# Performance work log

Hardware: AMD Instinct MI355X
Metric: run time of the kernel (lower is better)

## Reference

```python
import jax, jax.numpy as jnp
import numpy as np

NUM_E = 20000   # entities
NUM_R = 200     # relations (rel table has 2*NUM_R rows)
H = 200         # h_dim
TD = 48         # t_dim (UnionTimeEncode: two halves of 24)
HD = TD // 2
L_HIST = 32     # padded per-(batch,k) history list length
HIS_K = 3
N_HIST = 3      # len(his_list_g)
N_LAYERS = 2    # RGCN layers (config.num_layers)
E = 200000      # edges per historical graph
BATCH = 512


def setup_inputs() -> dict:
    key = jax.random.key(0)
    ks = jax.random.split(key, 32)
    nrm = lambda k, shape, s=0.05: (jax.random.normal(k, shape, jnp.float32) * s)
    inp = {}
    # graph / index inputs (int)
    inp['src'] = jax.random.randint(ks[0], (N_HIST, E), 0, NUM_E, jnp.int32)
    inp['dst'] = jax.random.randint(ks[1], (N_HIST, E), 0, NUM_E, jnp.int32)
    inp['etype'] = jax.random.randint(ks[2], (N_HIST, E), 0, 2 * NUM_R, jnp.int32)
    inp['data'] = jax.random.randint(ks[3], (BATCH, 4), 0, NUM_R, jnp.int32)  # s,r,o,t
    inp['his_idx'] = jax.random.randint(ks[4], (BATCH, HIS_K, L_HIST), 0, NUM_E, jnp.int32)
    inp['his_len'] = jax.random.randint(ks[5], (BATCH, HIS_K), 0, L_HIST + 1, jnp.int32)
    # parameters (float)
    inp['ent'] = nrm(ks[6], (NUM_E, H), 0.5)          # EntEmb.ent (normal init)
    inp['loop_weight'] = nrm(ks[7], (H, H))           # EntEmb self-loop weight
    inp['rel'] = nrm(ks[8], (2 * NUM_R, H), 0.5)
    # UnionTimeEncode params (AbsTimeEncode v=0 + CosTimeEncode)
    basis = (1.0 / 10 ** np.linspace(0.0, 9.0, HD)).astype(np.float32)
    inp['abs_freq'] = jnp.asarray(basis)
    inp['abs_phase'] = jnp.zeros((HD,), jnp.float32)
    inp['cos_freq'] = jnp.asarray(basis)
    inp['cos_phase'] = jnp.zeros((HD,), jnp.float32)
    # RGCN (RE-GCN style Union-RGCN layer: msg=(h_src+rel_e)@Wn, mean agg, self-loop)
    inp['Wn'] = nrm(ks[9], (N_LAYERS, H, H))
    inp['Ws'] = nrm(ks[10], (N_LAYERS, H, H))
    # GRUCell (PyTorch layout)
    inp['W_ih'] = nrm(ks[11], (3 * H, H + TD))
    inp['W_hh'] = nrm(ks[12], (3 * H, H))
    inp['b_ih'] = jnp.zeros((3 * H,), jnp.float32)
    inp['b_hh'] = jnp.zeros((3 * H,), jnp.float32)
    # attention fusion
    inp['Wb_w'] = nrm(ks[13], (H, 3 * H + TD))
    inp['Wb_b'] = jnp.zeros((H,), jnp.float32)
    inp['Wc_w'] = nrm(ks[14], (1, H))
    inp['Wc_b'] = jnp.zeros((1,), jnp.float32)
    # decoder (MLP query @ entity table)
    inp['Wd_w'] = nrm(ks[15], (H, 3 * H))
    inp['Wd_b'] = jnp.zeros((H,), jnp.float32)
    return inp


def _l2n(x, eps=1e-12):
    # F.normalize: x / max(||x||, eps)
    n = jnp.linalg.norm(x, axis=-1, keepdims=True)
    return x / jnp.maximum(n, eps)


def reference(src, dst, etype, data, his_idx, his_len,
              ent, loop_weight, rel, abs_freq, abs_phase, cos_freq, cos_phase,
              Wn, Ws, W_ih, W_hh, b_ih, b_hh, Wb_w, Wb_b, Wc_w, Wc_b, Wd_w, Wd_b):
    def tenc(t):  # t: [N,1] float -> [N,TD]
        a = jnp.tanh((t + 1.0) * abs_freq + abs_phase)   # AbsTimeEncode(act=tanh)
        c = jnp.cos(t * cos_freq + cos_phase)            # CosTimeEncode
        return jnp.concatenate([a, c], axis=1)

    s_i, r_i = data[:, 0], data[:, 1]
    ent_e = ent @ loop_weight                  # EntEmb self-loop (dropout=identity, eval)
    rel_n = _l2n(rel)
    prev = _l2n(ent_e)                         # g_list[0]
    tim_cnt = N_HIST
    ones_e = jnp.ones((E,), jnp.float32)
    for i in range(N_HIST):                    # python loop over fixed #graphs
        si, di, ei = src[i], dst[i], etype[i]
        deg = jax.ops.segment_sum(ones_e, di, num_segments=NUM_E)         # in-degree
        inv = 1.0 / jnp.maximum(deg, 1.0)
        # g.update_all(copy_src, mean): zero in-degree nodes -> 0
        agg = jax.ops.segment_sum(prev[si], di, num_segments=NUM_E) * inv[:, None]
        h = _l2n(jnp.where(deg[:, None] > 0, agg, 0.0))
        tim_cnt -= 1
        tim = jnp.where(deg > 0, float(tim_cnt), 100.0)[:, None]
        te = tenc(tim)                                                     # [NUM_E,TD]
        for l in range(N_LAYERS):              # RGCN
            msg = (h[si] + rel_n[ei]) @ Wn[l]                              # [E,H]
            nagg = jax.ops.segment_sum(msg, di, num_segments=NUM_E) * inv[:, None]
            h = jax.nn.relu(nagg + h @ Ws[l])
        h = _l2n(h)
        # GRUCell(cat([h, te]), prev)
        gi = jnp.concatenate([h, te], axis=1) @ W_ih.T + b_ih
        gh = prev @ W_hh.T + b_hh
        ir, iz, iN = jnp.split(gi, 3, axis=1)
        hr, hz, hN = jnp.split(gh, 3, axis=1)
        rg = jax.nn.sigmoid(ir + hr)
        zg = jax.nn.sigmoid(iz + hz)
        ng = jnp.tanh(iN + rg * hN)
        prev = _l2n((1.0 - zg) * ng + zg * prev)
    out = prev

    q_s, q_r = out[s_i], rel_n[r_i]
    tim_cnt = min(N_HIST, HIS_K)
    s_embs, atts = [], []
    pos = jnp.arange(L_HIST)[None, :]
    for k in range(min(N_HIST, HIS_K)):
        tim_cnt -= 1
        ln = his_len[:, k]
        mask = (pos < ln[:, None]).astype(jnp.float32)                     # [B,L]
        # sparse one-hot mm + divide by length
        tmp = jnp.einsum('blh,bl->bh', out[his_idx[:, k, :]], mask)
        tmp = _l2n(tmp / jnp.maximum(ln, 1).astype(jnp.float32)[:, None])
        tim = jnp.where(ln > 0, float(tim_cnt), 100.0)[:, None]
        te = tenc(tim)                                                     # [B,TD]
        s_embs.append(tmp)
        a = jax.nn.relu(jnp.concatenate([q_s, q_r, tmp, te], 1) @ Wb_w.T + Wb_b)
        atts.append(a @ Wc_w.T + Wc_b)                                     # [B,1]
    att = jax.nn.softmax(jnp.stack(atts, axis=1), axis=1)                  # [B,K,1]
    out2 = jnp.sum(jnp.stack(s_embs, axis=1) * att, axis=1)                # bmm fusion
    # decoder: MLP query scored against all entity states
    q = jax.nn.relu(jnp.concatenate([q_s, q_r, out2], 1) @ Wd_w.T + Wd_b)
    return q @ out.T                                                       # [B,NUM_E]
```

## Files before the change

kernel.cpp:

```cpp
#include <hip/hip_runtime.h>
#include <hip/hip_bf16.h>

#define NUM_E   20000
#define H_DIM   200
#define TD_DIM  48
#define HD_DIM  24
#define L_HIST  32
#define N_HIST  3
#define E_EDGES 200000
#define BATCH   512


__device__ inline float wave_sum64(float x) {
    #pragma unroll
    for (int m = 1; m < 64; m <<= 1) x += __shfl_xor(x, m);
    return x;
}

__device__ inline ushort f2bf(float f) {
    unsigned u = __float_as_uint(f);
    u += 0x7fffu + ((u >> 16) & 1u);
    return (ushort)(u >> 16);
}
__device__ inline float bf2f(ushort u) {
    return __uint_as_float(((unsigned)u) << 16);
}
__device__ inline float4 bf4_to_f4(ushort4 v) {
    return (float4){bf2f(v.x), bf2f(v.y), bf2f(v.z), bf2f(v.w)};
}

__global__ void fill_i32(int* __restrict__ p, long n, int v) {
    long i = (long)blockIdx.x * blockDim.x + threadIdx.x;
    if (i < n) p[i] = v;
}

__global__ void bias_sum(float* __restrict__ bsum, const float* __restrict__ b_ih,
                         const float* __restrict__ b_hh) {
    int j = blockIdx.x * 256 + threadIdx.x;
    if (j < 600) bsum[j] = b_ih[j] + b_hh[j];
}

__global__ void cvt_bf16_k(ushort* __restrict__ o, const float* __restrict__ in, long n) {
    long i = (long)blockIdx.x * 256 + threadIdx.x;
    if (i < n) o[i] = f2bf(in[i]);
}

__global__ void make_lo(ushort* __restrict__ lo, const float* __restrict__ x,
                        const ushort* __restrict__ hi, long n) {
    long i = (long)blockIdx.x * 256 + threadIdx.x;
    if (i < n) lo[i] = f2bf(x[i] - bf2f(hi[i]));
}

__global__ void tcvt_bf16_k(ushort* __restrict__ o, const float* __restrict__ in, int R, int C) {
    int i = blockIdx.x * 256 + threadIdx.x;
    if (i >= R * C) return;
    int r = i / C, c = i - r * C;
    o[(size_t)c * R + r] = f2bf(in[i]);
}

struct Segs {
    const float* A[4];
    const float* B[4];
    int lda[4], ldb[4], Ks[4];
    int nseg, Ktot;
};

__device__ inline void seg_find(const Segs& sg, int gk, int& s, int& loc) {
    s = 0; loc = gk;
    #pragma unroll
    for (int t = 0; t < 3; t++) {
        if (s + 1 < sg.nseg && loc >= sg.Ks[s]) { loc -= sg.Ks[s]; s++; }
    }
}

__global__ __launch_bounds__(256) void sgemm_splitk(
    float* __restrict__ P, const Segs sg, int M, int N, int nbx, int nby,
    int KS, int tpc)
{
    __shared__ float As[32][68];
    __shared__ float Bs[32][68];

    int tot = nbx * nby;
    int tot_all = tot * KS;
    int chunk = (tot_all + 7) >> 3;
    int v = (int)(blockIdx.x & 7) * chunk + (int)(blockIdx.x >> 3);
    if (v >= tot_all) return;
    int kc = v / tot;
    int tile = v - kc * tot;
    int by = tile / nbx, bx = tile - by * nbx;
    const int bn = bx * 64;
    const int bm = by * 64;
    const int tid = threadIdx.x;
    const int m0 = (tid >> 4) * 4;
    const int n0 = (tid & 15) * 4;

    float acc[4][4];
    #pragma unroll
    for (int i = 0; i < 4; i++)
        #pragma unroll
        for (int j = 0; j < 4; j++) acc[i][j] = 0.f;

    const int Ktot = sg.Ktot;
    const int ntile = (Ktot + 31) / 32;
    const int kt0 = kc * tpc;
    const int kt1 = min(ntile, kt0 + tpc);

    const int a_m  = tid & 31;
    const int a_k4 = (tid >> 5) * 4;
    const int b1_n = tid & 63;
    const int b1_k = (tid >> 6) * 4;

    float4 ra[2], rb[2];
    auto loadA = [&](int k0) {
        int gk = k0 + a_k4;
        bool kin = gk < Ktot;
        int s = 0, loc = 0;
        if (kin) seg_find(sg, gk, s, loc);
        const float* Ab = sg.A[s];
        const int lda = sg.lda[s];
        #pragma unroll
        for (int r = 0; r < 2; r++) {
            int row = bm + a_m + 32 * r;
            float4 vv = {0.f, 0.f, 0.f, 0.f};
            if (kin && row < M) vv = *(const float4*)(Ab + (size_t)row * lda + loc);
            ra[r] = vv;
        }
    };
    auto loadB = [&](int k0) {
        #pragma unroll
        for (int r = 0; r < 2; r++) {
            int k4 = b1_k + 16 * r;
            int gk = k0 + k4;
            bool kin = gk < Ktot;
            int s = 0, loc = 0;
            if (kin) seg_find(sg, gk, s, loc);
            const float* Bb = sg.B[s];
            const int ldb = sg.ldb[s];
            int gn = bn + b1_n;
            float4 vv = {0.f, 0.f, 0.f, 0.f};
            if (kin && gn < N) vv = *(const float4*)(Bb + (size_t)gn * ldb + loc);
            rb[r] = vv;
        }
    };

    if (kt0 < kt1) {
        loadA(kt0 * 32); loadB(kt0 * 32);
        for (int t = kt0; t < kt1; t++) {
            #pragma unroll
            for (int r = 0; r < 2; r++) {
                int m = a_m + 32 * r;
                As[a_k4 + 0][m] = ra[r].x;
                As[a_k4 + 1][m] = ra[r].y;
                As[a_k4 + 2][m] = ra[r].z;
                As[a_k4 + 3][m] = ra[r].w;
            }
            #pragma unroll
            for (int r = 0; r < 2; r++) {
                int k4 = b1_k + 16 * r;
                Bs[k4 + 0][b1_n] = rb[r].x;
                Bs[k4 + 1][b1_n] = rb[r].y;
                Bs[k4 + 2][b1_n] = rb[r].z;
                Bs[k4 + 3][b1_n] = rb[r].w;
            }
            __syncthreads();
            if (t + 1 < kt1) { loadA((t + 1) * 32); loadB((t + 1) * 32); }
            #pragma unroll 8
            for (int kk = 0; kk < 32; kk++) {
                float4 b = *(float4*)&Bs[kk][n0];
                float4 av = *(float4*)&As[kk][m0];
                float a[4] = {av.x, av.y, av.z, av.w};
                #pragma unroll
                for (int i = 0; i < 4; i++) {
                    acc[i][0] += a[i] * b.x;
                    acc[i][1] += a[i] * b.y;
                    acc[i][2] += a[i] * b.z;
                    acc[i][3] += a[i] * b.w;
                }
            }
            __syncthreads();
        }
    }

    int col = bn + n0;
    if (col < N) {
        #pragma unroll
        for (int i = 0; i < 4; i++) {
            int row = bm + m0 + i;
            if (row < M) {
                float4 o = {acc[i][0], acc[i][1], acc[i][2], acc[i][3]};
                *(float4*)(P + ((size_t)kc * M + row) * N + col) = o;
            }
        }
    }
}

__global__ void reduce_relu(float* __restrict__ out, const float* __restrict__ P,
                            const float* __restrict__ bias, int MN, int N, int KS)
{
    int i = blockIdx.x * 256 + threadIdx.x;
    if (i >= MN) return;
    float s = bias[i % N];
    for (int k = 0; k < KS; k++) s += P[(size_t)k * MN + i];
    out[i] = fmaxf(s, 0.f);
}

__global__ void reduce_relu_split(ushort* __restrict__ qhi, ushort* __restrict__ qlo,
                                  const float* __restrict__ P, const float* __restrict__ bias,
                                  int MN, int N, int KS)
{
    int i = blockIdx.x * 256 + threadIdx.x;
    if (i >= MN) return;
    float s = bias[i % N];
    for (int k = 0; k < KS; k++) s += P[(size_t)k * MN + i];
    s = fmaxf(s, 0.f);
    ushort h = f2bf(s);
    qhi[i] = h;
    qlo[i] = f2bf(s - bf2f(h));
}

typedef __attribute__((ext_vector_type(8))) short bfrag;
typedef __attribute__((ext_vector_type(4))) float ffrag;

struct BfSegs {
    const ushort* A[3];
    const ushort* B[3];
    int lda[3], ldb[3], Ks[3];
    int nseg, Ktot;
};

__device__ inline void bseg_find(const BfSegs& sg, int gk, int& s, int& loc) {
    s = 0; loc = gk;
    #pragma unroll
    for (int t = 0; t < 2; t++) {
        if (s + 1 < sg.nseg && loc >= sg.Ks[s]) { loc -= sg.Ks[s]; s++; }
    }
}

struct GemmDesc {
    BfSegs sg;
    float* C;
    ushort* Cb;
    const float* bias;
    int M, N, ldc;
    int act, flags, order;
    int nbx, nby, blk0, nblk;
};

struct MultiArgs {
    GemmDesc d[3];
    int nd;
    int tot;
};

template<int DI>
__device__ __forceinline__ void gemm_body(const MultiArgs& ma, int v,
                                          ushort* __restrict__ Als,
                                          ushort* __restrict__ Bls)
{
    const GemmDesc& D = ma.d[DI];
    const BfSegs& sg = D.sg;
    const int tile = v - D.blk0;
    int by, bx;
    if (D.order == 0) { by = tile / D.nbx; bx = tile - by * D.nbx; }
    else              { bx = tile / D.nby; by = tile - bx * D.nby; }
    const int bm = by * 64, bn = bx * 64;
    const int M = D.M, N = D.N;

    const int tid  = threadIdx.x;
    const int lane = tid & 63;
    const int w    = tid >> 6;
    const int wm   = (w & 1) * 2;
    const int wn   = (w >> 1) * 2;

    ffrag acc[2][2];
    #pragma unroll
    for (int i = 0; i < 2; i++)
        #pragma unroll
        for (int j = 0; j < 2; j++) acc[i][j] = (ffrag){0.f, 0.f, 0.f, 0.f};

    const int Ktot = sg.Ktot;
    const int nkt = (Ktot + 63) >> 6;

    int a_m[2], a_kq[2], a_wc[2];
    #pragma unroll
    for (int i = 0; i < 2; i++) {
        int c = i * 256 + tid;
        a_m[i] = c & 63; a_kq[i] = c >> 6;
        a_wc[i] = ((a_m[i] >> 4) * 2 + (a_kq[i] >> 2)) * 64 + (a_kq[i] & 3) * 16 + (a_m[i] & 15);
    }
    int b_n[2], b_kq[2], b_wc[2];
    #pragma unroll
    for (int i = 0; i < 2; i++) {
        int c = i * 256 + tid;
        b_n[i] = c & 63; b_kq[i] = c >> 6;
        b_wc[i] = ((b_n[i] >> 4) * 2 + (b_kq[i] >> 2)) * 64 + (b_kq[i] & 3) * 16 + (b_n[i] & 15);
    }

    uint4 ra[2], rb[2];
    auto loadA = [&](int k0) {
        #pragma unroll
        for (int i = 0; i < 2; i++) {
            int gk = k0 + a_kq[i] * 8;
            int row = bm + a_m[i];
            uint4 vv = {0u, 0u, 0u, 0u};
            if (gk < Ktot && row < M) {
                int s, loc; bseg_find(sg, gk, s, loc);
                vv = *(const uint4*)(sg.A[s] + (size_t)row * sg.lda[s] + loc);
            }
            ra[i] = vv;
        }
    };
    auto loadB = [&](int k0) {
        #pragma unroll
        for (int i = 0; i < 2; i++) {
            int gk = k0 + b_kq[i] * 8;
            int gn = bn + b_n[i];
            uint4 vv = {0u, 0u, 0u, 0u};
            if (gk < Ktot && gn < N) {
                int s, loc; bseg_find(sg, gk, s, loc);
                vv = *(const uint4*)(sg.B[s] + (size_t)gn * sg.ldb[s] + loc);
            }
            rb[i] = vv;
        }
    };

    loadA(0); loadB(0);

    for (int t = 0; t < nkt; t++) {
        #pragma unroll
        for (int i = 0; i < 2; i++) *(uint4*)(&Als[a_wc[i] * 8]) = ra[i];
        #pragma unroll
        for (int i = 0; i < 2; i++) *(uint4*)(&Bls[b_wc[i] * 8]) = rb[i];
        __syncthreads();

        if (t + 1 < nkt) { loadA((t + 1) << 6); loadB((t + 1) << 6); }

        #pragma unroll
        for (int kt = 0; kt < 2; kt++) {
            bfrag af[2], bf[2];
            #pragma unroll
            for (int i = 0; i < 2; i++)
                af[i] = *(const bfrag*)(&Als[(((wm + i) * 2 + kt) * 64 + lane) * 8]);
            #pragma unroll
            for (int j = 0; j < 2; j++)
                bf[j] = *(const bfrag*)(&Bls[(((wn + j) * 2 + kt) * 64 + lane) * 8]);
            #pragma unroll
            for (int i = 0; i < 2; i++)
                #pragma unroll
                for (int j = 0; j < 2; j++)
                    acc[i][j] = __builtin_amdgcn_mfma_f32_16x16x32_bf16(af[i], bf[j], acc[i][j], 0, 0, 0);
        }
        __syncthreads();
    }

    const int rbase = (lane >> 4) * 4;
    const int cl = lane & 15;
    #pragma unroll
    for (int j = 0; j < 2; j++) {
        int col = bn + (wn + j) * 16 + cl;
        if (col >= N) continue;
        float bv = D.bias ? D.bias[col] : 0.f;
        #pragma unroll
        for (int i = 0; i < 2; i++) {
            int mrow = bm + (wm + i) * 16 + rbase;
            #pragma unroll
            for (int r = 0; r < 4; r++) {
                int row = mrow + r;
                if (row < M) {
                    float o = acc[i][j][r] + bv;
                    if (D.act == 1) o = fmaxf(o, 0.f);
                    else if (D.act == 2) o = 1.f / (1.f + expf(-o));
                    if (D.flags & 1) D.C[(size_t)row * D.ldc + col] = o;
                    if (D.flags & 2) D.Cb[(size_t)row * D.ldc + col] = f2bf(o);
                }
            }
        }
    }
}

__global__ __launch_bounds__(256) void mfma_multi(MultiArgs ma)
{
    __shared__ __align__(16) ushort Als[4096];
    __shared__ __align__(16) ushort Bls[4096];

    int tot = ma.tot;
    int chunk = (tot + 7) >> 3;
    int v = (int)(blockIdx.x & 7) * chunk + (int)(blockIdx.x >> 3);
    if (v >= tot) return;

    int di = 0;
    if (ma.nd > 1 && v >= ma.d[1].blk0) di = 1;
    if (ma.nd > 2 && v >= ma.d[2].blk0) di = 2;

    if (di == 0)      gemm_body<0>(ma, v, Als, Bls);
    else if (di == 1) gemm_body<1>(ma, v, Als, Bls);
    else              gemm_body<2>(ma, v, Als, Bls);
}


__global__ void count_dst3(const int* __restrict__ dst, int* __restrict__ cnt) {
    long e = (long)blockIdx.x * 256 + threadIdx.x;
    if (e < (long)N_HIST * E_EDGES) {
        int g = (int)(e / E_EDGES);
        atomicAdd(&cnt[g * NUM_E + dst[e]], 1);
    }
}

__global__ __launch_bounds__(1024) void scan_rows3(
    const int* __restrict__ cnt_all, int* __restrict__ row_start_all,
    int* __restrict__ cursor_all, float* __restrict__ degf_all,
    float* __restrict__ invd_all)
{
    __shared__ int part[1024];
    const int g = blockIdx.x;
    const int* cnt = cnt_all + g * NUM_E;
    int* row_start  = row_start_all + g * (NUM_E + 4);
    int* cursor     = cursor_all + g * NUM_E;
    float* degf     = degf_all + g * NUM_E;
    float* invd     = invd_all + g * NUM_E;

    const int CH = (NUM_E + 1023) / 1024;
    int t = threadIdx.x;
    int base = t * CH;
    int local[32];
    int s = 0;
    for (int j = 0; j < CH; j++) {
        int idx = base + j;
        int c = (idx < NUM_E) ? cnt[idx] : 0;
        local[j] = s; s += c;
    }
    part[t] = s;
    __syncthreads();
    for (int off = 1; off < 1024; off <<= 1) {
        int vv = (t >= off) ? part[t - off] : 0;
        __syncthreads();
        part[t] += vv;
        __syncthreads();
    }
    int pre = (t == 0) ? 0 : part[t - 1];
    for (int j = 0; j < CH; j++) {
        int idx = base + j;
        if (idx < NUM_E) {
            int rs = pre + local[j];
            row_start[idx] = rs;
            cursor[idx] = rs;
            int c = cnt[idx];
            degf[idx] = (float)c;
            invd[idx] = 1.f / fmaxf((float)c, 1.f);
        }
    }
    if (t == 1023) row_start[NUM_E] = part[1023];
}

__global__ void build_perm3(const int* __restrict__ src, const int* __restrict__ dst,
                            const int* __restrict__ etype, int* __restrict__ cursor_all,
                            int* __restrict__ ssrc_all, int* __restrict__ setype_all)
{
    long e = (long)blockIdx.x * 256 + threadIdx.x;
    if (e >= (long)N_HIST * E_EDGES) return;
    int g = (int)(e / E_EDGES);
    int pos = atomicAdd(&cursor_all[g * NUM_E + dst[e]], 1);
    ssrc_all[(long)g * E_EDGES + pos]   = src[e];
    setype_all[(long)g * E_EDGES + pos] = etype[e];
}


__global__ __launch_bounds__(256) void seg_gather_norm_bf(
    ushort* __restrict__ bh, const ushort* __restrict__ bprev,
    const int* __restrict__ ssrc, const int* __restrict__ row_start,
    const float* __restrict__ invd)
{
    int v = blockIdx.x * 4 + (threadIdx.x >> 6);
    int lane = threadIdx.x & 63;
    if (v >= NUM_E) return;
    int s0 = row_start[v], s1 = row_start[v + 1];
    bool act = lane < 50;
    float4 acc = {0.f, 0.f, 0.f, 0.f};
    int j = s0;
    for (; j + 1 < s1; j += 2) {
        int sa = ssrc[j], sb = ssrc[j + 1];
        if (act) {
            float4 xa = bf4_to_f4(*(const ushort4*)(bprev + (long)sa * H_DIM + lane * 4));
            float4 xb = bf4_to_f4(*(const ushort4*)(bprev + (long)sb * H_DIM + lane * 4));
            acc.x += xa.x + xb.x; acc.y += xa.y + xb.y;
            acc.z += xa.z + xb.z; acc.w += xa.w + xb.w;
        }
    }
    if (j < s1) {
        int sa = ssrc[j];
        if (act) {
            float4 xa = bf4_to_f4(*(const ushort4*)(bprev + (long)sa * H_DIM + lane * 4));
            acc.x += xa.x; acc.y += xa.y; acc.z += xa.z; acc.w += xa.w;
        }
    }
    float iv = invd[v];
    acc.x *= iv; acc.y *= iv; acc.z *= iv; acc.w *= iv;
    float ss = act ? (acc.x*acc.x + acc.y*acc.y + acc.z*acc.z + acc.w*acc.w) : 0.f;
    ss = wave_sum64(ss);
    float r = 1.f / fmaxf(sqrtf(ss), 1e-12f);
    if (act) {
        ushort4 ob = {f2bf(acc.x * r), f2bf(acc.y * r), f2bf(acc.z * r), f2bf(acc.w * r)};
        *(ushort4*)(bh + (long)v * H_DIM + lane * 4) = ob;
    }
}

__global__ __launch_bounds__(256) void seg_gather_layer_bf(
    ushort* __restrict__ btmp, const ushort* __restrict__ bh, const ushort* __restrict__ brel,
    const int* __restrict__ ssrc, const int* __restrict__ setype,
    const int* __restrict__ row_start, const float* __restrict__ invd)
{
    int v = blockIdx.x * 4 + (threadIdx.x >> 6);
    int lane = threadIdx.x & 63;
    if (v >= NUM_E) return;
    int s0 = row_start[v], s1 = row_start[v + 1];
    bool act = lane < 50;
    float4 acc = {0.f, 0.f, 0.f, 0.f};
    int j = s0;
    for (; j + 1 < s1; j += 2) {
        int sa = ssrc[j], ta = setype[j];
        int sb = ssrc[j + 1], tb = setype[j + 1];
        if (act) {
            float4 xa = bf4_to_f4(*(const ushort4*)(bh   + (long)sa * H_DIM + lane * 4));
            float4 ya = bf4_to_f4(*(const ushort4*)(brel + (long)ta * H_DIM + lane * 4));
            float4 xb = bf4_to_f4(*(const ushort4*)(bh   + (long)sb * H_DIM + lane * 4));
            float4 yb = bf4_to_f4(*(const ushort4*)(brel + (long)tb * H_DIM + lane * 4));
            acc.x += (xa.x + ya.x) + (xb.x + yb.x);
            acc.y += (xa.y + ya.y) + (xb.y + yb.y);
            acc.z += (xa.z + ya.z) + (xb.z + yb.z);
            acc.w += (xa.w + ya.w) + (xb.w + yb.w);
        }
    }
    if (j < s1) {
        int s = ssrc[j];
        int t = setype[j];
        if (act) {
            float4 x = bf4_to_f4(*(const ushort4*)(bh   + (long)s * H_DIM + lane * 4));
            float4 y = bf4_to_f4(*(const ushort4*)(brel + (long)t * H_DIM + lane * 4));
            acc.x += x.x + y.x; acc.y += x.y + y.y;
            acc.z += x.z + y.z; acc.w += x.w + y.w;
        }
    }
    float iv = invd[v];
    if (act) {
        ushort4 ob = {f2bf(acc.x * iv), f2bf(acc.y * iv), f2bf(acc.z * iv), f2bf(acc.w * iv)};
        *(ushort4*)(btmp + (long)v * H_DIM + lane * 4) = ob;
    }
}


__global__ __launch_bounds__(256) void l2norm_rows4(
    float* __restrict__ out, ushort* __restrict__ bout,
    const float* __restrict__ in, int nrows)
{
    int v = blockIdx.x * 4 + (threadIdx.x >> 6);
    int lane = threadIdx.x & 63;
    if (v >= nrows) return;
    bool act = lane < 50;
    float4 x = {0.f, 0.f, 0.f, 0.f};
    if (act) x = *(const float4*)(in + (long)v * H_DIM + lane * 4);
    float ss = x.x*x.x + x.y*x.y + x.z*x.z + x.w*x.w;
    ss = wave_sum64(ss);
    float r = 1.f / fmaxf(sqrtf(ss), 1e-12f);
    if (act) {
        long base = (long)v * H_DIM + lane * 4;
        float4 o = {x.x * r, x.y * r, x.z * r, x.w * r};
        *(float4*)(out + base) = o;
        if (bout) {
            ushort4 ob = {f2bf(o.x), f2bf(o.y), f2bf(o.z), f2bf(o.w)};
            *(ushort4*)(bout + base) = ob;
        }
    }
}

__global__ __launch_bounds__(256) void l2norm_bf4(ushort* __restrict__ b, int nrows)
{
    int v = blockIdx.x * 4 + (threadIdx.x >> 6);
    int lane = threadIdx.x & 63;
    if (v >= nrows) return;
    bool act = lane < 50;
    float4 x = {0.f, 0.f, 0.f, 0.f};
    long base = (long)v * H_DIM + lane * 4;
    if (act) x = bf4_to_f4(*(const ushort4*)(b + base));
    float ss = x.x*x.x + x.y*x.y + x.z*x.z + x.w*x.w;
    ss = wave_sum64(ss);
    float r = 1.f / fmaxf(sqrtf(ss), 1e-12f);
    if (act) {
        ushort4 ob = {f2bf(x.x * r), f2bf(x.y * r), f2bf(x.z * r), f2bf(x.w * r)};
        *(ushort4*)(b + base) = ob;
    }
}

__global__ void tenc_table3(ushort* __restrict__ tbl, const float* __restrict__ af,
                            const float* __restrict__ ap, const float* __restrict__ cf,
                            const float* __restrict__ cp)
{
    int j = blockIdx.x * 256 + threadIdx.x;
    if (j >= 384) return;
    int g = j >> 7;
    int r = j & 127;
    int half = r >> 6;
    int jj = r & 63;
    if (jj >= TD_DIM) return;
    float tcnt = (float)(N_HIST - 1 - g);
    float t = half ? 100.0f : tcnt;
    float val;
    if (jj < HD_DIM) val = tanhf((t + 1.f) * af[jj] + ap[jj]);
    else             val = cosf(t * cf[jj - HD_DIM] + cp[jj - HD_DIM]);
    tbl[g * 128 + half * 64 + jj] = f2bf(val);
}

__global__ void tenc_fill3(ushort* __restrict__ bte3, const float* __restrict__ degf_all,
                           const ushort* __restrict__ tbl)
{
    long idx = (long)blockIdx.x * 256 + threadIdx.x;
    if (idx >= (long)N_HIST * NUM_E * 6) return;
    int g = (int)(idx / (NUM_E * 6));
    int rem = (int)(idx - (long)g * NUM_E * 6);
    int v = rem / 6, c = rem - v * 6;
    int base = (degf_all[g * NUM_E + v] > 0.f) ? 0 : 64;
    *(uint4*)(bte3 + ((long)g * NUM_E + v) * TD_DIM + c * 8) =
        *(const uint4*)(tbl + g * 128 + base + c * 8);
}

__global__ __launch_bounds__(256) void gru_fused(
    float* __restrict__ prev, ushort* __restrict__ bprev, const float* __restrict__ rz,
    const float* __restrict__ iN, const float* __restrict__ hN)
{
    int v = blockIdx.x * 4 + (threadIdx.x >> 6);
    int lane = threadIdx.x & 63;
    if (v >= NUM_E) return;
    bool act = lane < 50;
    long b200 = (long)v * H_DIM + lane * 4;
    long b400 = (long)v * 400 + lane * 4;
    float4 o = {0.f, 0.f, 0.f, 0.f};
    if (act) {
        float4 r4 = *(const float4*)(rz + b400);
        float4 z4 = *(const float4*)(rz + b400 + 200);
        float4 n4 = *(const float4*)(iN + b200);
        float4 g4 = *(const float4*)(hN + b200);
        float4 p4 = *(const float4*)(prev + b200);
        float ngx = tanhf(n4.x + r4.x * g4.x);
        float ngy = tanhf(n4.y + r4.y * g4.y);
        float ngz = tanhf(n4.z + r4.z * g4.z);
        float ngw = tanhf(n4.w + r4.w * g4.w);
        o.x = (1.f - z4.x) * ngx + z4.x * p4.x;
        o.y = (1.f - z4.y) * ngy + z4.y * p4.y;
        o.z = (1.f - z4.z) * ngz + z4.z * p4.z;
        o.w = (1.f - z4.w) * ngw + z4.w * p4.w;
    }
    float ss = o.x*o.x + o.y*o.y + o.z*o.z + o.w*o.w;
    ss = wave_sum64(ss);
    float r = 1.f / fmaxf(sqrtf(ss), 1e-12f);
    if (act) {
        float4 wv = {o.x * r, o.y * r, o.z * r, o.w * r};
        *(float4*)(prev + b200) = wv;
        ushort4 ob = {f2bf(wv.x), f2bf(wv.y), f2bf(wv.z), f2bf(wv.w)};
        *(ushort4*)(bprev + b200) = ob;
    }
}


__global__ void gather_qs_qr3(float* __restrict__ qs3, float* __restrict__ qr3,
                              const float* __restrict__ out, const float* __restrict__ reln,
                              const int* __restrict__ data)
{
    long i = (long)blockIdx.x * 256 + threadIdx.x;
    if (i >= (long)BATCH * H_DIM) return;
    int b = (int)(i / H_DIM), j = (int)(i % H_DIM);
    float vs = out[(long)data[b * 4 + 0] * H_DIM + j];
    float vr = reln[(long)data[b * 4 + 1] * H_DIM + j];
    const long S = (long)BATCH * H_DIM;
    qs3[i] = vs; qs3[i + S] = vs; qs3[i + 2*S] = vs;
    qr3[i] = vr; qr3[i + S] = vr; qr3[i + 2*S] = vr;
}

__global__ __launch_bounds__(64) void semb_kernel(
    float* __restrict__ semb, const float* __restrict__ out,
    const int* __restrict__ his_idx, const int* __restrict__ his_len)
{
    int b = blockIdx.x, k = blockIdx.y;
    int lane = threadIdx.x;
    int ln = his_len[b * 3 + k];
    if (ln > L_HIST) ln = L_HIST;
    float vals[4] = {0.f, 0.f, 0.f, 0.f};
    for (int l = 0; l < ln; l++) {
        int idx = his_idx[((long)b * 3 + k) * L_HIST + l];
        #pragma unroll
        for (int t = 0; t < 4; t++) {
            int j = lane + t * 64;
            if (j < H_DIM) vals[t] += out[(long)idx * H_DIM + j];
        }
    }
    float scale = 1.f / fmaxf((float)ln, 1.f);
    float ss = 0.f;
    #pragma unroll
    for (int t = 0; t < 4; t++) { vals[t] *= scale; ss += vals[t] * vals[t]; }
    ss = wave_sum64(ss);
    float r = 1.f / fmaxf(sqrtf(ss), 1e-12f);
    #pragma unroll
    for (int t = 0; t < 4; t++) {
        int j = lane + t * 64;
        if (j < H_DIM) semb[((long)k * BATCH + b) * H_DIM + j] = vals[t] * r;
    }
}

__global__ void tenc_batch(float* __restrict__ teb, const int* __restrict__ his_len,
                           const float* __restrict__ af, const float* __restrict__ ap,
                           const float* __restrict__ cf, const float* __restrict__ cp)
{
    int idx = blockIdx.x * 256 + threadIdx.x;
    if (idx >= 3 * BATCH * TD_DIM) return;
    int k = idx / (BATCH * TD_DIM);
    int rem = idx - k * (BATCH * TD_DIM);
    int b = rem / TD_DIM, j = rem % TD_DIM;
    int ln = his_len[b * 3 + k];
    float t = (ln > 0) ? (float)(2 - k) : 100.0f;
    float val;
    if (j < HD_DIM) val = tanhf((t + 1.f) * af[j] + ap[j]);
    else            val = cosf(t * cf[j - HD_DIM] + cp[j - HD_DIM]);
    teb[idx] = val;
}

__global__ __launch_bounds__(256) void att_logits_rows(
    float* __restrict__ atts, const float* __restrict__ a,
    const float* __restrict__ Wc_w, const float* __restrict__ Wc_b)
{
    int row = blockIdx.x * 4 + (threadIdx.x >> 6);
    int lane = threadIdx.x & 63;
    if (row >= 3 * BATCH) return;
    int k = row >> 9;
    int b = row & 511;
    float s = 0.f;
    for (int j = lane; j < H_DIM; j += 64) s += a[(long)row * H_DIM + j] * Wc_w[j];
    s = wave_sum64(s);
    if (lane == 0) atts[b * 3 + k] = s + Wc_b[0];
}

__global__ void softmax_out2(float* __restrict__ out2, const float* __restrict__ atts,
                             const float* __restrict__ semb)
{
    long i = (long)blockIdx.x * 256 + threadIdx.x;
    if (i >= (long)BATCH * H_DIM) return;
    int b = (int)(i / H_DIM), j = (int)(i % H_DIM);
    float l0 = atts[b * 3 + 0], l1 = atts[b * 3 + 1], l2 = atts[b * 3 + 2];
    float m = fmaxf(l0, fmaxf(l1, l2));
    float e0 = expf(l0 - m), e1 = expf(l1 - m), e2 = expf(l2 - m);
    float s = e0 + e1 + e2;
    float v = (e0 * semb[((long)0 * BATCH + b) * H_DIM + j] +
               e1 * semb[((long)1 * BATCH + b) * H_DIM + j] +
               e2 * semb[((long)2 * BATCH + b) * H_DIM + j]) / s;
    out2[i] = v;
}


extern "C" void kernel_launch(void* const* d_in, const int* in_sizes, int n_in,
                              void* d_out, int out_size, void* d_ws, size_t ws_size,
                              hipStream_t stream)
{
    (void)in_sizes; (void)n_in; (void)out_size; (void)ws_size;

    const int*   src     = (const int*)d_in[0];
    const int*   dst     = (const int*)d_in[1];
    const int*   etype   = (const int*)d_in[2];
    const int*   data    = (const int*)d_in[3];
    const int*   his_idx = (const int*)d_in[4];
    const int*   his_len = (const int*)d_in[5];
    const float* ent     = (const float*)d_in[6];
    const float* loop_w  = (const float*)d_in[7];
    const float* rel     = (const float*)d_in[8];
    const float* af      = (const float*)d_in[9];
    const float* ap      = (const float*)d_in[10];
    const float* cf      = (const float*)d_in[11];
    const float* cp      = (const float*)d_in[12];
    const float* Wn      = (const float*)d_in[13];
    const float* Ws      = (const float*)d_in[14];
    const float* W_ih    = (const float*)d_in[15];
    const float* W_hh    = (const float*)d_in[16];
    const float* b_ih    = (const float*)d_in[17];
    const float* b_hh    = (const float*)d_in[18];
    const float* Wb_w    = (const float*)d_in[19];
    const float* Wb_b    = (const float*)d_in[20];
    const float* Wc_w    = (const float*)d_in[21];
    const float* Wc_b    = (const float*)d_in[22];
    const float* Wd_w    = (const float*)d_in[23];
    const float* Wd_b    = (const float*)d_in[24];
    float* out_p = (float*)d_out;

    float* wp = (float*)d_ws;
    size_t off = 0;
    auto alloc = [&](size_t n) {
        size_t n4 = (n + 3) & ~(size_t)3;
        float* p = wp + off; off += n4; return p;
    };
    const long nE200 = (long)NUM_E * H_DIM;
    float* prev   = alloc(nE200);
    float* h1     = alloc(nE200);
    float* tmp    = alloc(nE200);
    float* rz     = out_p;
    ushort* bh0   = (ushort*)alloc(nE200 / 2);
    ushort* bh1   = (ushort*)alloc(nE200 / 2);
    ushort* btmp  = (ushort*)alloc(nE200 / 2);
    ushort* bprev = (ushort*)alloc(nE200 / 2);
    ushort* plo   = (ushort*)alloc(nE200 / 2);
    ushort* bte3  = (ushort*)alloc((size_t)N_HIST * NUM_E * TD_DIM / 2);
    ushort* brel  = (ushort*)alloc(400 * H_DIM / 2);
    ushort* bW_ih = (ushort*)alloc(600 * 248 / 2);
    ushort* bW_hh = (ushort*)alloc(600 * 200 / 2);
    ushort* bWn_t = (ushort*)alloc(2 * 200 * 200 / 2);
    ushort* bWs_t = (ushort*)alloc(2 * 200 * 200 / 2);
    ushort* bLp_t = (ushort*)alloc(200 * 200 / 2);
    ushort* qhi   = (ushort*)alloc(BATCH * H_DIM / 2);
    ushort* qlo   = (ushort*)alloc(BATCH * H_DIM / 2);
    ushort* ttbl  = (ushort*)alloc(256);
    float* degf   = alloc(3 * NUM_E);
    float* invd   = alloc(3 * NUM_E);
    float* reln   = alloc(400 * H_DIM);
    float* bsum   = alloc(1024);
    float* qs3    = alloc(3 * BATCH * H_DIM);
    float* qr3    = alloc(3 * BATCH * H_DIM);
    float* semb   = alloc(3 * BATCH * H_DIM);
    float* teb    = alloc(3 * BATCH * TD_DIM);
    float* abuf   = alloc(3 * BATCH * H_DIM);
    float* atts   = alloc(2048);
    float* out2   = alloc(BATCH * H_DIM);
    int* cnt       = (int*)alloc(3 * NUM_E);
    int* row_start = (int*)alloc(3 * (NUM_E + 4));
    int* cursor    = (int*)alloc(3 * NUM_E);
    int* ssrc      = (int*)alloc(3L * E_EDGES);
    int* setype    = (int*)alloc(3L * E_EDGES);

    auto nblk = [](long n) { return (unsigned)((n + 255) / 256); };

    auto bseg1 = [](const ushort* A, int la, const ushort* B, int lb, int K) {
        BfSegs s{}; s.A[0]=A; s.lda[0]=la; s.B[0]=B; s.ldb[0]=lb; s.Ks[0]=K;
        s.nseg=1; s.Ktot=K; return s;
    };
    auto bseg2 = [](const ushort* A0, int la0, const ushort* B0, int lb0, int K0,
                    const ushort* A1, int la1, const ushort* B1, int lb1, int K1) {
        BfSegs s{}; s.A[0]=A0; s.lda[0]=la0; s.B[0]=B0; s.ldb[0]=lb0; s.Ks[0]=K0;
        s.A[1]=A1; s.lda[1]=la1; s.B[1]=B1; s.ldb[1]=lb1; s.Ks[1]=K1;
        s.nseg=2; s.Ktot=K0+K1; return s;
    };
    auto bseg3 = [](const ushort* A0, int la0, const ushort* B0, int lb0, int K0,
                    const ushort* A1, int la1, const ushort* B1, int lb1, int K1,
                    const ushort* A2, int la2, const ushort* B2, int lb2, int K2) {
        BfSegs s{}; s.A[0]=A0; s.lda[0]=la0; s.B[0]=B0; s.ldb[0]=lb0; s.Ks[0]=K0;
        s.A[1]=A1; s.lda[1]=la1; s.B[1]=B1; s.ldb[1]=lb1; s.Ks[1]=K1;
        s.A[2]=A2; s.lda[2]=la2; s.B[2]=B2; s.ldb[2]=lb2; s.Ks[2]=K2;
        s.nseg=3; s.Ktot=K0+K1+K2; return s;
    };

    auto desc = [](const BfSegs& sg, float* C, ushort* Cb, const float* bias,
                   int M, int N, int ldc, int act, int flags, int order) {
        GemmDesc D{}; D.sg=sg; D.C=C; D.Cb=Cb; D.bias=bias;
        D.M=M; D.N=N; D.ldc=ldc; D.act=act; D.flags=flags; D.order=order;
        D.nbx=(N+63)>>6; D.nby=(M+63)>>6; D.nblk=D.nbx*D.nby; D.blk0=0;
        return D;
    };
    auto launch_multi = [&](GemmDesc* ds, int nd) {
        MultiArgs ma{};
        int tot = 0;
        for (int i = 0; i < nd; i++) { ds[i].blk0 = tot; tot += ds[i].nblk; ma.d[i] = ds[i]; }
        ma.nd = nd; ma.tot = tot;
        unsigned grid = (unsigned)(((tot + 7) >> 3) << 3);
        mfma_multi<<<grid, 256, 0, stream>>>(ma);
    };

    auto seg3 = [](const float* A0, int la0, const float* B0, int lb0, int K0,
                   const float* A1, int la1, const float* B1, int lb1, int K1,
                   const float* A2, int la2, const float* B2, int lb2, int K2) {
        Segs s{}; s.A[0]=A0; s.lda[0]=la0; s.B[0]=B0; s.ldb[0]=lb0; s.Ks[0]=K0;
        s.A[1]=A1; s.lda[1]=la1; s.B[1]=B1; s.ldb[1]=lb1; s.Ks[1]=K1;
        s.A[2]=A2; s.lda[2]=la2; s.B[2]=B2; s.ldb[2]=lb2; s.Ks[2]=K2;
        s.nseg=3; s.Ktot=K0+K1+K2; return s;
    };
    auto seg4 = [](const float* A0, int la0, const float* B0, int lb0, int K0,
                   const float* A1, int la1, const float* B1, int lb1, int K1,
                   const float* A2, int la2, const float* B2, int lb2, int K2,
                   const float* A3, int la3, const float* B3, int lb3, int K3) {
        Segs s{}; s.A[0]=A0; s.lda[0]=la0; s.B[0]=B0; s.ldb[0]=lb0; s.Ks[0]=K0;
        s.A[1]=A1; s.lda[1]=la1; s.B[1]=B1; s.ldb[1]=lb1; s.Ks[1]=K1;
        s.A[2]=A2; s.lda[2]=la2; s.B[2]=B2; s.ldb[2]=lb2; s.Ks[2]=K2;
        s.A[3]=A3; s.lda[3]=la3; s.B[3]=B3; s.ldb[3]=lb3; s.Ks[3]=K3;
        s.nseg=4; s.Ktot=K0+K1+K2+K3; return s;
    };
    auto splitk = [&](float* P, const Segs& sg, int M, int N, int KS) {
        int nbx = (N + 63) >> 6;
        int nby = (M + 63) >> 6;
        int ntile = (sg.Ktot + 31) / 32;
        int tpc = (ntile + KS - 1) / KS;
        int tot_all = nbx * nby * KS;
        unsigned grid = (unsigned)(((tot_all + 7) >> 3) << 3);
        sgemm_splitk<<<grid, 256, 0, stream>>>(P, sg, M, N, nbx, nby, KS, tpc);
    };

    const unsigned r4 = (NUM_E + 3) / 4;

    l2norm_rows4<<<100, 256, 0, stream>>>(reln, brel, rel, 400);
    bias_sum<<<3, 256, 0, stream>>>(bsum, b_ih, b_hh);
    cvt_bf16_k<<<nblk(600L*248), 256, 0, stream>>>(bW_ih, W_ih, 600L*248);
    cvt_bf16_k<<<nblk(600L*200), 256, 0, stream>>>(bW_hh, W_hh, 600L*200);
    tcvt_bf16_k<<<nblk(40000), 256, 0, stream>>>(bLp_t, loop_w, 200, 200);
    tcvt_bf16_k<<<nblk(40000), 256, 0, stream>>>(bWn_t,          Wn,          200, 200);
    tcvt_bf16_k<<<nblk(40000), 256, 0, stream>>>(bWn_t + 40000,  Wn + 40000,  200, 200);
    tcvt_bf16_k<<<nblk(40000), 256, 0, stream>>>(bWs_t,          Ws,          200, 200);
    tcvt_bf16_k<<<nblk(40000), 256, 0, stream>>>(bWs_t + 40000,  Ws + 40000,  200, 200);

    fill_i32<<<nblk(3L * NUM_E), 256, 0, stream>>>(cnt, 3L * NUM_E, 0);
    count_dst3<<<nblk(3L * E_EDGES), 256, 0, stream>>>(dst, cnt);
    scan_rows3<<<3, 1024, 0, stream>>>(cnt, row_start, cursor, degf, invd);
    build_perm3<<<nblk(3L * E_EDGES), 256, 0, stream>>>(src, dst, etype, cursor, ssrc, setype);
    tenc_table3<<<2, 256, 0, stream>>>(ttbl, af, ap, cf, cp);
    tenc_fill3<<<nblk(3L * NUM_E * 6), 256, 0, stream>>>(bte3, degf, ttbl);

    cvt_bf16_k<<<nblk(nE200), 256, 0, stream>>>(btmp, ent, nE200);
    {
        GemmDesc d0 = desc(bseg1(btmp, H_DIM, bLp_t, H_DIM, H_DIM),
                           tmp, nullptr, nullptr, NUM_E, H_DIM, H_DIM, 0, 1, 0);
        launch_multi(&d0, 1);
    }
    l2norm_rows4<<<r4, 256, 0, stream>>>(prev, bprev, tmp, NUM_E);

    for (int i = 0; i < N_HIST; i++) {
        const int* ssrc_g = ssrc + (long)i * E_EDGES;
        const int* sety_g = setype + (long)i * E_EDGES;
        const int* rs_g   = row_start + i * (NUM_E + 4);
        const float* iv_g = invd + i * NUM_E;
        ushort* bte_g     = bte3 + (long)i * NUM_E * TD_DIM;

        seg_gather_norm_bf<<<r4, 256, 0, stream>>>(bh0, bprev, ssrc_g, rs_g, iv_g);

        seg_gather_layer_bf<<<r4, 256, 0, stream>>>(btmp, bh0, brel, ssrc_g, sety_g, rs_g, iv_g);
        {
            GemmDesc d0 = desc(bseg2(btmp, H_DIM, bWn_t,         H_DIM, H_DIM,
                                     bh0,  H_DIM, bWs_t,         H_DIM, H_DIM),
                               nullptr, bh1, nullptr, NUM_E, H_DIM, H_DIM, 1, 2, 0);
            launch_multi(&d0, 1);
        }
        seg_gather_layer_bf<<<r4, 256, 0, stream>>>(btmp, bh1, brel, ssrc_g, sety_g, rs_g, iv_g);
        {
            GemmDesc d0 = desc(bseg2(btmp, H_DIM, bWn_t + 40000, H_DIM, H_DIM,
                                     bh1,  H_DIM, bWs_t + 40000, H_DIM, H_DIM),
                               nullptr, bh0, nullptr, NUM_E, H_DIM, H_DIM, 1, 2, 0);
            launch_multi(&d0, 1);
        }
        l2norm_bf4<<<r4, 256, 0, stream>>>(bh0, NUM_E);

        {
            GemmDesc d3[3];
            d3[0] = desc(bseg3(bh0,   H_DIM,  bW_ih,       248, H_DIM,
                               bte_g, TD_DIM, bW_ih + 200, 248, TD_DIM,
                               bprev, H_DIM,  bW_hh,       200, H_DIM),
                         rz, nullptr, bsum, NUM_E, 400, 400, 2, 1, 0);
            d3[1] = desc(bseg2(bh0,   H_DIM,  bW_ih + 400*248,       248, H_DIM,
                               bte_g, TD_DIM, bW_ih + 400*248 + 200, 248, TD_DIM),
                         h1, nullptr, b_ih + 400, NUM_E, H_DIM, H_DIM, 0, 1, 0);
            d3[2] = desc(bseg1(bprev, H_DIM, bW_hh + 400*200, 200, H_DIM),
                         tmp, nullptr, b_hh + 400, NUM_E, H_DIM, H_DIM, 0, 1, 0);
            launch_multi(d3, 3);
        }

        gru_fused<<<r4, 256, 0, stream>>>(prev, bprev, rz, h1, tmp);
    }

    gather_qs_qr3<<<nblk((long)BATCH * H_DIM), 256, 0, stream>>>(qs3, qr3, prev, reln, data);
    semb_kernel<<<dim3(BATCH, 3), 64, 0, stream>>>(semb, prev, his_idx, his_len);
    tenc_batch<<<nblk(3L * BATCH * TD_DIM), 256, 0, stream>>>(teb, his_len, af, ap, cf, cp);

    {
        const int KS = 8;
        const int MN = 3 * BATCH * H_DIM;
        splitk(h1, seg4(qs3, H_DIM,  Wb_w,       648, H_DIM,
                        qr3, H_DIM,  Wb_w + 200, 648, H_DIM,
                        semb, H_DIM, Wb_w + 400, 648, H_DIM,
                        teb, TD_DIM, Wb_w + 600, 648, TD_DIM),
               3 * BATCH, H_DIM, KS);
        reduce_relu<<<nblk(MN), 256, 0, stream>>>(abuf, h1, Wb_b, MN, H_DIM, KS);
    }
    att_logits_rows<<<(3 * BATCH + 3) / 4, 256, 0, stream>>>(atts, abuf, Wc_w, Wc_b);
    softmax_out2<<<nblk((long)BATCH * H_DIM), 256, 0, stream>>>(out2, atts, semb);

    {
        const int KS = 8;
        const int MN = BATCH * H_DIM;
        splitk(tmp, seg3(qs3, H_DIM,  Wd_w,       600, H_DIM,
                         qr3, H_DIM,  Wd_w + 200, 600, H_DIM,
                         out2, H_DIM, Wd_w + 400, 600, H_DIM),
               BATCH, H_DIM, KS);
        reduce_relu_split<<<nblk(MN), 256, 0, stream>>>(qhi, qlo, tmp, Wd_b, MN, H_DIM, KS);
    }

    make_lo<<<nblk(nE200), 256, 0, stream>>>(plo, prev, bprev, nE200);

    {
        GemmDesc d0 = desc(bseg3(qhi, H_DIM, bprev, H_DIM, H_DIM,
                                 qhi, H_DIM, plo,   H_DIM, H_DIM,
                                 qlo, H_DIM, bprev, H_DIM, H_DIM),
                           out_p, nullptr, nullptr, BATCH, NUM_E, NUM_E, 0, 1, 1);
        launch_multi(&d0, 1);
    }
}
```

Baseline: 1.096 ms.

## Split GEMM block tiles into independent per-wave 32x32 tiles without barriers

Replaces the 64x64 block tile, which four waves computed cooperatively with shared LDS and __syncthreads, with independent 32x32 tiles, each owned by one wave with its own LDS region. This removes block-level barriers and yields four times as many tiles, giving better load balance and more parallelism for the small-M GEMMs. In exchange, each tile reuses less data, so global loads per FLOP roughly double. Waves sharing a block no longer share A or B loads, and LDS per block doubles to 32KB.

```diff
diff --git a/kernel.cpp b/kernel.cpp
--- a/kernel.cpp
+++ b/kernel.cpp
@@ -253,24 +253,19 @@
 };
 
 template<int DI>
-__device__ __forceinline__ void gemm_body(const MultiArgs& ma, int v,
+__device__ __forceinline__ void gemm_wave(const MultiArgs& ma, int gw,
                                           ushort* __restrict__ Als,
                                           ushort* __restrict__ Bls)
 {
     const GemmDesc& D = ma.d[DI];
     const BfSegs& sg = D.sg;
-    const int tile = v - D.blk0;
-    int by, bx;
-    if (D.order == 0) { by = tile / D.nbx; bx = tile - by * D.nbx; }
-    else              { bx = tile / D.nby; by = tile - bx * D.nby; }
-    const int bm = by * 64, bn = bx * 64;
+    const int t0 = gw - D.blk0;
+    int my, mx;
+    if (D.order == 0) { my = t0 / D.nbx; mx = t0 - my * D.nbx; }
+    else              { mx = t0 / D.nby; my = t0 - mx * D.nby; }
+    const int bm = my * 32, bn = mx * 32;
     const int M = D.M, N = D.N;
-
-    const int tid  = threadIdx.x;
-    const int lane = tid & 63;
-    const int w    = tid >> 6;
-    const int wm   = (w & 1) * 2;
-    const int wn   = (w >> 1) * 2;
+    const int lane = (int)(threadIdx.x & 63);
 
     ffrag acc[2][2];
     #pragma unroll
@@ -281,27 +276,20 @@
     const int Ktot = sg.Ktot;
     const int nkt = (Ktot + 63) >> 6;
 
-    int a_m[2], a_kq[2], a_wc[2];
+    int s_m[4], s_kq[4], s_wc[4];
     #pragma unroll
-    for (int i = 0; i < 2; i++) {
-        int c = i * 256 + tid;
-        a_m[i] = c & 63; a_kq[i] = c >> 6;
-        a_wc[i] = ((a_m[i] >> 4) * 2 + (a_kq[i] >> 2)) * 64 + (a_kq[i] & 3) * 16 + (a_m[i] & 15);
-    }
-    int b_n[2], b_kq[2], b_wc[2];
-    #pragma unroll
-    for (int i = 0; i < 2; i++) {
-        int c = i * 256 + tid;
-        b_n[i] = c & 63; b_kq[i] = c >> 6;
-        b_wc[i] = ((b_n[i] >> 4) * 2 + (b_kq[i] >> 2)) * 64 + (b_kq[i] & 3) * 16 + (b_n[i] & 15);
-    }
-
-    uint4 ra[2], rb[2];
+    for (int i = 0; i < 4; i++) {
+        int c = i * 64 + lane;
+        s_m[i] = c >> 3; s_kq[i] = c & 7;
+        s_wc[i] = ((s_m[i] >> 4) * 2 + (s_kq[i] >> 2)) * 64 + (s_kq[i] & 3) * 16 + (s_m[i] & 15);
+    }
+
+    uint4 ra[4], rb[4];
     auto loadA = [&](int k0) {
         #pragma unroll
-        for (int i = 0; i < 2; i++) {
-            int gk = k0 + a_kq[i] * 8;
-            int row = bm + a_m[i];
+        for (int i = 0; i < 4; i++) {
+            int gk = k0 + s_kq[i] * 8;
+            int row = bm + s_m[i];
             uint4 vv = {0u, 0u, 0u, 0u};
             if (gk < Ktot && row < M) {
                 int s, loc; bseg_find(sg, gk, s, loc);
@@ -312,9 +300,9 @@
     };
     auto loadB = [&](int k0) {
         #pragma unroll
-        for (int i = 0; i < 2; i++) {
-            int gk = k0 + b_kq[i] * 8;
-            int gn = bn + b_n[i];
+        for (int i = 0; i < 4; i++) {
+            int gk = k0 + s_kq[i] * 8;
+            int gn = bn + s_m[i];
             uint4 vv = {0u, 0u, 0u, 0u};
             if (gk < Ktot && gn < N) {
                 int s, loc; bseg_find(sg, gk, s, loc);
@@ -328,10 +316,9 @@
 
     for (int t = 0; t < nkt; t++) {
         #pragma unroll
-        for (int i = 0; i < 2; i++) *(uint4*)(&Als[a_wc[i] * 8]) = ra[i];
-        #pragma unroll
-        for (int i = 0; i < 2; i++) *(uint4*)(&Bls[b_wc[i] * 8]) = rb[i];
-        __syncthreads();
+        for (int i = 0; i < 4; i++) *(uint4*)(&Als[s_wc[i] * 8]) = ra[i];
+        #pragma unroll
+        for (int i = 0; i < 4; i++) *(uint4*)(&Bls[s_wc[i] * 8]) = rb[i];
 
         if (t + 1 < nkt) { loadA((t + 1) << 6); loadB((t + 1) << 6); }
 
@@ -340,29 +327,28 @@
             bfrag af[2], bf[2];
             #pragma unroll
             for (int i = 0; i < 2; i++)
-                af[i] = *(const bfrag*)(&Als[(((wm + i) * 2 + kt) * 64 + lane) * 8]);
+                af[i] = *(const bfrag*)(&Als[((i * 2 + kt) * 64 + lane) * 8]);
             #pragma unroll
             for (int j = 0; j < 2; j++)
-                bf[j] = *(const bfrag*)(&Bls[(((wn + j) * 2 + kt) * 64 + lane) * 8]);
+                bf[j] = *(const bfrag*)(&Bls[((j * 2 + kt) * 64 + lane) * 8]);
             #pragma unroll
             for (int i = 0; i < 2; i++)
                 #pragma unroll
                 for (int j = 0; j < 2; j++)
                     acc[i][j] = __builtin_amdgcn_mfma_f32_16x16x32_bf16(af[i], bf[j], acc[i][j], 0, 0, 0);
         }
-        __syncthreads();
     }
 
     const int rbase = (lane >> 4) * 4;
     const int cl = lane & 15;
     #pragma unroll
     for (int j = 0; j < 2; j++) {
-        int col = bn + (wn + j) * 16 + cl;
+        int col = bn + j * 16 + cl;
         if (col >= N) continue;
         float bv = D.bias ? D.bias[col] : 0.f;
         #pragma unroll
         for (int i = 0; i < 2; i++) {
-            int mrow = bm + (wm + i) * 16 + rbase;
+            int mrow = bm + i * 16 + rbase;
             #pragma unroll
             for (int r = 0; r < 4; r++) {
                 int row = mrow + r;
@@ -380,21 +366,27 @@
 
 __global__ __launch_bounds__(256) void mfma_multi(MultiArgs ma)
 {
-    __shared__ __align__(16) ushort Als[4096];
-    __shared__ __align__(16) ushort Bls[4096];
+    __shared__ __align__(16) ushort lds[16384];
+
+    const int w = (int)(threadIdx.x >> 6);
+    ushort* Als = lds + w * 4096;
+    ushort* Bls = Als + 2048;
 
     int tot = ma.tot;
-    int chunk = (tot + 7) >> 3;
+    int nblk = (tot + 3) >> 2;
+    int chunk = (nblk + 7) >> 3;
     int v = (int)(blockIdx.x & 7) * chunk + (int)(blockIdx.x >> 3);
-    if (v >= tot) return;
+    if (v >= nblk) return;
+    int gw = v * 4 + w;
+    if (gw >= tot) return;
 
     int di = 0;
-    if (ma.nd > 1 && v >= ma.d[1].blk0) di = 1;
-    if (ma.nd > 2 && v >= ma.d[2].blk0) di = 2;
-
-    if (di == 0)      gemm_body<0>(ma, v, Als, Bls);
-    else if (di == 1) gemm_body<1>(ma, v, Als, Bls);
-    else              gemm_body<2>(ma, v, Als, Bls);
+    if (ma.nd > 1 && gw >= ma.d[1].blk0) di = 1;
+    if (ma.nd > 2 && gw >= ma.d[2].blk0) di = 2;
+
+    if (di == 0)      gemm_wave<0>(ma, gw, Als, Bls);
+    else if (di == 1) gemm_wave<1>(ma, gw, Als, Bls);
+    else              gemm_wave<2>(ma, gw, Als, Bls);
 }
 
 
@@ -854,7 +846,7 @@
                    int M, int N, int ldc, int act, int flags, int order) {
         GemmDesc D{}; D.sg=sg; D.C=C; D.Cb=Cb; D.bias=bias;
         D.M=M; D.N=N; D.ldc=ldc; D.act=act; D.flags=flags; D.order=order;
-        D.nbx=(N+63)>>6; D.nby=(M+63)>>6; D.nblk=D.nbx*D.nby; D.blk0=0;
+        D.nbx=(N+31)>>5; D.nby=(M+31)>>5; D.nblk=D.nbx*D.nby; D.blk0=0;
         return D;
     };
     auto launch_multi = [&](GemmDesc* ds, int nd) {
@@ -862,7 +854,8 @@
         int tot = 0;
         for (int i = 0; i < nd; i++) { ds[i].blk0 = tot; tot += ds[i].nblk; ma.d[i] = ds[i]; }
         ma.nd = nd; ma.tot = tot;
-        unsigned grid = (unsigned)(((tot + 7) >> 3) << 3);
+        unsigned blocks = (unsigned)((tot + 3) >> 2);
+        unsigned grid = ((blocks + 7) >> 3) << 3;
         mfma_multi<<<grid, 256, 0, stream>>>(ma);
     };
 
```

Measured after the change: 1.523 ms. +39.0%, slower.
